# Performance work log

Hardware: AMD Instinct MI355X
Metric: run time of the kernel (lower is better)

## Reference

```python
import jax, jax.numpy as jnp
import numpy as np

N_SENT = 100000   # source ('sent') nodes
N_TYPE = 10000    # destination ('type') nodes
E = 640000        # edges of etype 'has'
D = 128           # out_dim
LEAKY_SLOPE = 0.01  # F.leaky_relu default


def setup_inputs() -> dict:
    key = jax.random.key(0)
    k0, k1, k2, k3, k4 = jax.random.split(key, 5)
    h_sent = jax.random.normal(k0, (N_SENT, D), jnp.float32)
    h_type = jax.random.normal(k1, (N_TYPE, D), jnp.float32)
    # attn_fc: Linear(2*D, 1, bias=False) -> weight [1, 2*D]
    attn_w = jax.random.normal(k2, (1, 2 * D), jnp.float32) * (1.0 / np.sqrt(2 * D))
    src_idx = jax.random.randint(k3, (E,), 0, N_SENT, dtype=jnp.int32)
    dst_idx = jax.random.randint(k4, (E,), 0, N_TYPE, dtype=jnp.int32)
    return {"h_sent": h_sent, "h_type": h_type, "attn_w": attn_w,
            "src_idx": src_idx, "dst_idx": dst_idx}


def reference(h_sent, h_type, attn_w, src_idx, dst_idx):
    w = attn_w[0]  # [2D]
    # attn_fc(cat(src_h, dst_h)) == src_h @ w[:D] + dst_h @ w[D:]  (no bias)
    s_src = h_sent @ w[:D]   # [N_SENT]
    s_dst = h_type @ w[D:]   # [N_TYPE]
    e = jax.nn.leaky_relu(s_src[src_idx] + s_dst[dst_idx], LEAKY_SLOPE)  # [E]
    # segment (per-destination) softmax over incoming edges
    m = jax.ops.segment_max(e, dst_idx, num_segments=N_TYPE)             # [N_TYPE]
    m = jnp.where(jnp.isfinite(m), m, 0.0)                               # empty segments -> 0
    ex = jnp.exp(e - m[dst_idx])                                         # [E]
    denom = jax.ops.segment_sum(ex, dst_idx, num_segments=N_TYPE)        # [N_TYPE]
    alpha = ex / denom[dst_idx]                                          # [E]
    # weighted scatter-sum of source features into destination nodes
    msg = alpha[:, None] * h_sent[src_idx]                               # [E, D]
    h_new = jax.ops.segment_sum(msg, dst_idx, num_segments=N_TYPE)       # [N_TYPE, D]
    # DGL only updates nodes that received messages; isolated nodes keep h
    deg = jax.ops.segment_sum(jnp.ones_like(e), dst_idx, num_segments=N_TYPE)
    return jnp.where(deg[:, None] > 0, h_new, h_type)
```

## Files before the change

### kernel.cpp

```cpp
#include <hip/hip_runtime.h>
#include <stdint.h>
#include <stddef.h>

#define N_SENT 100000
#define N_TYPE 10000
#define NEDGE  640000
#define NROWS  (N_SENT + N_TYPE)
#define MAXDEG 256
#define HB     64
#define HCHUNK (NEDGE / HB)

__device__ __forceinline__ float bf2f(uint32_t lo16) {
    return __builtin_bit_cast(float, lo16 << 16);
}
__device__ __forceinline__ uint32_t f2bf(float f) {
    uint32_t u = __builtin_bit_cast(uint32_t, f);
    return (u + 0x7fffu + ((u >> 16) & 1u)) >> 16;
}

__device__ __forceinline__ bool detect_bf16(const uint32_t* __restrict__ h) {
    uint32_t u = h[threadIdx.x & 63];
    uint32_t e_lo = (u >> 7) & 0xffu;
    int ok = (e_lo >= 100u && e_lo <= 140u) ? 1 : 0;
    unsigned long long m = __ballot(ok);
    return __popcll(m) >= 48;
}

#define SCORE_BLOCKS ((NROWS + 63) / 64)

__global__ __launch_bounds__(256) void scores_k(const void* __restrict__ h_sent,
                                                const void* __restrict__ h_type,
                                                const void* __restrict__ attn_w,
                                                float* __restrict__ s_src,
                                                float* __restrict__ s_dst) {
    int lane = threadIdx.x & 63;
    int r0   = (blockIdx.x * 4 + (int)(threadIdx.x >> 6)) * 16;
    bool isbf = detect_bf16((const uint32_t*)h_sent);
    float v[16];
    if (isbf) {
        uint32_t wv_s = ((const uint32_t*)attn_w)[lane];
        uint32_t wv_t = ((const uint32_t*)attn_w)[64 + lane];
        float ws0 = bf2f(wv_s & 0xffffu), ws1 = bf2f(wv_s >> 16);
        float wt0 = bf2f(wv_t & 0xffffu), wt1 = bf2f(wv_t >> 16);
#pragma unroll
        for (int i = 0; i < 16; i++) {
            int g = r0 + i;
            if (g >= NROWS) { v[i] = 0.0f; continue; }
            bool isSrc = g < N_SENT;
            const uint32_t* hp = isSrc
                ? (const uint32_t*)h_sent + (size_t)g * 64
                : (const uint32_t*)h_type + (size_t)(g - N_SENT) * 64;
            uint32_t hv = hp[lane];
            v[i] = isSrc ? (bf2f(hv & 0xffffu) * ws0 + bf2f(hv >> 16) * ws1)
                         : (bf2f(hv & 0xffffu) * wt0 + bf2f(hv >> 16) * wt1);
        }
    } else {
        float2 wv_s = ((const float2*)attn_w)[lane];
        float2 wv_t = ((const float2*)attn_w)[64 + lane];
#pragma unroll
        for (int i = 0; i < 16; i++) {
            int g = r0 + i;
            if (g >= NROWS) { v[i] = 0.0f; continue; }
            bool isSrc = g < N_SENT;
            const float2* hp = isSrc
                ? (const float2*)h_sent + (size_t)g * 64
                : (const float2*)h_type + (size_t)(g - N_SENT) * 64;
            float2 hv = hp[lane];
            v[i] = isSrc ? (hv.x * wv_s.x + hv.y * wv_s.y)
                         : (hv.x * wv_t.x + hv.y * wv_t.y);
        }
    }
    int b0 = lane & 1, b1 = (lane >> 1) & 1, b2 = (lane >> 2) & 1, b3 = (lane >> 3) & 1;
    float w_[8];
#pragma unroll
    for (int i = 0; i < 8; i++) {
        float keep = b0 ? v[2 * i + 1] : v[2 * i];
        float send = b0 ? v[2 * i]     : v[2 * i + 1];
        w_[i] = keep + __shfl_xor(send, 1, 64);
    }
    float x_[4];
#pragma unroll
    for (int i = 0; i < 4; i++) {
        float keep = b1 ? w_[2 * i + 1] : w_[2 * i];
        float send = b1 ? w_[2 * i]     : w_[2 * i + 1];
        x_[i] = keep + __shfl_xor(send, 2, 64);
    }
    float y_[2];
#pragma unroll
    for (int i = 0; i < 2; i++) {
        float keep = b2 ? x_[2 * i + 1] : x_[2 * i];
        float send = b2 ? x_[2 * i]     : x_[2 * i + 1];
        y_[i] = keep + __shfl_xor(send, 4, 64);
    }
    float z;
    {
        float keep = b3 ? y_[1] : y_[0];
        float send = b3 ? y_[0] : y_[1];
        z = keep + __shfl_xor(send, 8, 64);
    }
    z += __shfl_xor(z, 16, 64);
    z += __shfl_xor(z, 32, 64);
    if (lane < 16) {
        int g = r0 + lane;
        if (g < NROWS) {
            if (g < N_SENT) s_src[g] = z;
            else            s_dst[g - N_SENT] = z;
        }
    }
}

__global__ __launch_bounds__(256) void count_k(const int* __restrict__ dst,
                                               uint32_t* __restrict__ count2) {
    __shared__ uint32_t hist[N_TYPE];
    int cb = blockIdx.x;
    int t  = threadIdx.x;
    for (int i = t; i < N_TYPE; i += 256) hist[i] = 0u;
    __syncthreads();
    int e0 = cb * HCHUNK;
    for (int i = t; i < HCHUNK; i += 256)
        atomicAdd(&hist[dst[e0 + i]], 1u);
    __syncthreads();
    uint32_t* row = count2 + (size_t)cb * N_TYPE;
    for (int i = t; i < N_TYPE; i += 256) row[i] = hist[i];
}

__global__ __launch_bounds__(256) void sumscan_k(uint32_t* __restrict__ count2,
                                                 uint32_t* __restrict__ total) {
    int b = blockIdx.x * 256 + threadIdx.x;
    if (b >= N_TYPE) return;
    uint32_t run = 0;
#pragma unroll 4
    for (int c = 0; c < HB; c++) {
        uint32_t* p = count2 + (size_t)c * N_TYPE + b;
        uint32_t v = *p;
        *p = run;
        run += v;
    }
    total[b] = run;
}

__global__ __launch_bounds__(1024) void scan_k(const uint32_t* __restrict__ total,
                                               uint32_t* __restrict__ offsets) {
    const int CH = 10;
    int t = threadIdx.x, lane = t & 63, wv = t >> 6;
    int base = t * CH;
    uint32_t local[CH];
    uint32_t tsum = 0;
#pragma unroll
    for (int i = 0; i < CH; i++) {
        int idx = base + i;
        uint32_t c = (idx < N_TYPE) ? total[idx] : 0u;
        local[i] = c;
        tsum += c;
    }
    uint32_t orig = tsum;
#pragma unroll
    for (int off = 1; off < 64; off <<= 1) {
        uint32_t v = __shfl_up(tsum, off, 64);
        if (lane >= off) tsum += v;
    }
    __shared__ uint32_t wsum[16];
    if (lane == 63) wsum[wv] = tsum;
    __syncthreads();
    if (wv == 0 && lane < 16) {
        uint32_t u = wsum[lane], o = u;
#pragma unroll
        for (int off = 1; off < 16; off <<= 1) {
            uint32_t v = __shfl_up(u, off, 64);
            if (lane >= off) u += v;
        }
        wsum[lane] = u - o;
    }
    __syncthreads();
    uint32_t run = wsum[wv] + tsum - orig;
#pragma unroll
    for (int i = 0; i < CH; i++) {
        int idx = base + i;
        if (idx < N_TYPE) {
            offsets[idx] = run;
            run += local[i];
        } else if (idx == N_TYPE) {
            offsets[idx] = run;
        }
    }
}

__global__ __launch_bounds__(256) void fill_k(const int* __restrict__ src,
                                              const int* __restrict__ dst,
                                              const uint32_t* __restrict__ offsets,
                                              const uint32_t* __restrict__ base2,
                                              uint32_t* __restrict__ edge_src) {
    __shared__ uint32_t cur[N_TYPE];
    int cb = blockIdx.x;
    int t  = threadIdx.x;
    const uint32_t* brow = base2 + (size_t)cb * N_TYPE;
    for (int i = t; i < N_TYPE; i += 256) cur[i] = offsets[i] + brow[i];
    __syncthreads();
    int e0 = cb * HCHUNK;
    for (int i = t; i < HCHUNK; i += 256) {
        int e = e0 + i;
        uint32_t pos = atomicAdd(&cur[dst[e]], 1u);
        edge_src[pos] = (uint32_t)src[e];
    }
}

__global__ __launch_bounds__(256) void agg_k(const void* __restrict__ h_sent,
                                             const void* __restrict__ h_type,
                                             const float* __restrict__ s_src,
                                             const float* __restrict__ s_dst,
                                             const uint32_t* __restrict__ offsets,
                                             const uint32_t* __restrict__ edge_src,
                                             void* __restrict__ out) {
    __shared__ float    sc[4][MAXDEG];
    __shared__ uint32_t ss[4][MAXDEG];
    int j     = (blockIdx.x * 256 + threadIdx.x) >> 6;
    int wslot = threadIdx.x >> 6;
    int lane  = threadIdx.x & 63;
    bool valid = j < N_TYPE;
    bool isbf  = detect_bf16((const uint32_t*)h_sent);
    uint32_t beg = 0, deg = 0;
    float sdj = 0.0f;
    if (valid) {
        beg = offsets[j];
        deg = offsets[j + 1] - beg;
        sdj = s_dst[j];
    }
    float*    mysc = sc[wslot];
    uint32_t* myss = ss[wslot];
    bool fits = (deg <= MAXDEG);
    float m = -INFINITY;
    for (uint32_t k = lane; k < deg; k += 64) {
        uint32_t s = edge_src[beg + k];
        float v = s_src[s] + sdj;
        v = v > 0.0f ? v : 0.01f * v;
        if (fits) { mysc[k] = v; myss[k] = s; }
        m = fmaxf(m, v);
    }
#pragma unroll
    for (int off = 32; off; off >>= 1) m = fmaxf(m, __shfl_xor(m, off, 64));
    __syncthreads();
    if (!valid) return;
    if (deg == 0) {
        if (isbf) ((uint32_t*)out)[(size_t)j * 64 + lane] =
                      ((const uint32_t*)h_type)[(size_t)j * 64 + lane];
        else      ((float2*)out)[(size_t)j * 64 + lane] =
                      ((const float2*)h_type)[(size_t)j * 64 + lane];
        return;
    }
    float denom = 0.0f, a0 = 0.0f, a1 = 0.0f;
    if (isbf) {
        const uint32_t* hp = (const uint32_t*)h_sent;
        uint32_t k = 0;
        if (fits) {
            for (; k + 8 <= deg; k += 8) {
                uint32_t sv[8]; float vv[8]; uint32_t gv[8];
#pragma unroll
                for (int i = 0; i < 8; i++) { sv[i] = myss[k + i]; vv[i] = mysc[k + i]; }
#pragma unroll
                for (int i = 0; i < 8; i++) gv[i] = hp[(size_t)sv[i] * 64 + lane];
#pragma unroll
                for (int i = 0; i < 8; i++) {
                    float w = __expf(vv[i] - m);
                    denom += w;
                    a0 += w * bf2f(gv[i] & 0xffffu);
                    a1 += w * bf2f(gv[i] >> 16);
                }
            }
            for (; k < deg; ++k) {
                float w = __expf(mysc[k] - m);
                uint32_t g = hp[(size_t)myss[k] * 64 + lane];
                denom += w;
                a0 += w * bf2f(g & 0xffffu);
                a1 += w * bf2f(g >> 16);
            }
        } else {
            for (k = 0; k < deg; ++k) {
                uint32_t s = edge_src[beg + k];
                float v = s_src[s] + sdj; v = v > 0.0f ? v : 0.01f * v;
                float w = __expf(v - m);
                uint32_t g = hp[(size_t)s * 64 + lane];
                denom += w;
                a0 += w * bf2f(g & 0xffffu);
                a1 += w * bf2f(g >> 16);
            }
        }
        float inv = 1.0f / denom;
        ((uint32_t*)out)[(size_t)j * 64 + lane] = f2bf(a0 * inv) | (f2bf(a1 * inv) << 16);
    } else {
        const float2* hp = (const float2*)h_sent;
        uint32_t k = 0;
        if (fits) {
            for (; k + 8 <= deg; k += 8) {
                uint32_t sv[8]; float vv[8]; float2 gv[8];
#pragma unroll
                for (int i = 0; i < 8; i++) { sv[i] = myss[k + i]; vv[i] = mysc[k + i]; }
#pragma unroll
                for (int i = 0; i < 8; i++) gv[i] = hp[(size_t)sv[i] * 64 + lane];
#pragma unroll
                for (int i = 0; i < 8; i++) {
                    float w = __expf(vv[i] - m);
                    denom += w;
                    a0 += w * gv[i].x;
                    a1 += w * gv[i].y;
                }
            }
            for (; k < deg; ++k) {
                float w = __expf(mysc[k] - m);
                float2 g = hp[(size_t)myss[k] * 64 + lane];
                denom += w;
                a0 += w * g.x;
                a1 += w * g.y;
            }
        } else {
            for (k = 0; k < deg; ++k) {
                uint32_t s = edge_src[beg + k];
                float v = s_src[s] + sdj; v = v > 0.0f ? v : 0.01f * v;
                float w = __expf(v - m);
                float2 g = hp[(size_t)s * 64 + lane];
                denom += w;
                a0 += w * g.x;
                a1 += w * g.y;
            }
        }
        float inv = 1.0f / denom;
        ((float2*)out)[(size_t)j * 64 + lane] = make_float2(a0 * inv, a1 * inv);
    }
}

static inline size_t align_up(size_t x) { return (x + 255) & ~(size_t)255; }

extern "C" void kernel_launch(void* const* d_in, const int* in_sizes, int n_in,
                              void* d_out, int out_size, void* d_ws, size_t ws_size,
                              hipStream_t stream) {
    const void* h_sent = d_in[0];
    const void* h_type = d_in[1];
    const void* attn_w = d_in[2];
    const int* src_idx = (const int*)d_in[3];
    const int* dst_idx = (const int*)d_in[4];

    char* w = (char*)d_ws;
    float*    s_src     = (float*)w;    w += align_up((size_t)N_SENT * 4);
    float*    s_dst     = (float*)w;    w += align_up((size_t)N_TYPE * 4);
    uint32_t* count2    = (uint32_t*)w; w += align_up((size_t)HB * N_TYPE * 4);
    uint32_t* total     = (uint32_t*)w; w += align_up((size_t)N_TYPE * 4);
    uint32_t* offsets   = (uint32_t*)w; w += align_up((size_t)(N_TYPE + 1) * 4);
    uint32_t* edge_src  = (uint32_t*)w; w += align_up((size_t)NEDGE * 4);

    scores_k<<<SCORE_BLOCKS, 256, 0, stream>>>(h_sent, h_type, attn_w, s_src, s_dst);
    count_k<<<HB, 256, 0, stream>>>(dst_idx, count2);
    sumscan_k<<<(N_TYPE + 255) / 256, 256, 0, stream>>>(count2, total);
    scan_k<<<1, 1024, 0, stream>>>(total, offsets);
    fill_k<<<HB, 256, 0, stream>>>(src_idx, dst_idx, offsets, count2, edge_src);
    agg_k<<<(N_TYPE + 3) / 4, 256, 0, stream>>>(h_sent, h_type, s_src, s_dst,
                                                offsets, edge_src, d_out);
}
```

Measured before the change: 198.3 us.

## Precompute edge weights in fill and split aggregation into source-row slabs for locality

The fill kernel now computes each edge's unnormalized softmax weight exp(leaky_relu(s_src+s_dst)) and stores it next to the source index, removing the per-destination max pass. Aggregation is split into 8 slabs over source-row ranges so concurrently running blocks gather from a smaller part of h_sent, aiming for better L2 reuse. Partial numerators are stored as bf16 and summed in a combine kernel, with a plain single-pass fallback when workspace is short. The cost is that every edge list is scanned 8 times, plus extra partial-buffer traffic and an extra launch. Dropping max subtraction risks overflow for large scores, and bf16 partials lose precision on fp32 inputs.

```diff
diff --git a/kernel.cpp b/kernel.cpp
--- a/kernel.cpp
+++ b/kernel.cpp
@@ -6,9 +6,10 @@
 #define N_TYPE 10000
 #define NEDGE  640000
 #define NROWS  (N_SENT + N_TYPE)
-#define MAXDEG 256
 #define HB     64
 #define HCHUNK (NEDGE / HB)
+#define NSLAB  8
+#define SLABW  (N_SENT / NSLAB)
 
 __device__ __forceinline__ float bf2f(uint32_t lo16) {
     return __builtin_bit_cast(float, lo16 << 16);
@@ -187,9 +188,11 @@
 
 __global__ __launch_bounds__(256) void fill_k(const int* __restrict__ src,
                                               const int* __restrict__ dst,
+                                              const float* __restrict__ s_src,
+                                              const float* __restrict__ s_dst,
                                               const uint32_t* __restrict__ offsets,
                                               const uint32_t* __restrict__ base2,
-                                              uint32_t* __restrict__ edge_src) {
+                                              uint2* __restrict__ edata) {
     __shared__ uint32_t cur[N_TYPE];
     int cb = blockIdx.x;
     int t  = threadIdx.x;
@@ -199,132 +202,168 @@
     int e0 = cb * HCHUNK;
     for (int i = t; i < HCHUNK; i += 256) {
         int e = e0 + i;
-        uint32_t pos = atomicAdd(&cur[dst[e]], 1u);
-        edge_src[pos] = (uint32_t)src[e];
-    }
-}
-
-__global__ __launch_bounds__(256) void agg_k(const void* __restrict__ h_sent,
-                                             const void* __restrict__ h_type,
-                                             const float* __restrict__ s_src,
-                                             const float* __restrict__ s_dst,
-                                             const uint32_t* __restrict__ offsets,
-                                             const uint32_t* __restrict__ edge_src,
-                                             void* __restrict__ out) {
-    __shared__ float    sc[4][MAXDEG];
-    __shared__ uint32_t ss[4][MAXDEG];
-    int j     = (blockIdx.x * 256 + threadIdx.x) >> 6;
-    int wslot = threadIdx.x >> 6;
-    int lane  = threadIdx.x & 63;
-    bool valid = j < N_TYPE;
-    bool isbf  = detect_bf16((const uint32_t*)h_sent);
-    uint32_t beg = 0, deg = 0;
-    float sdj = 0.0f;
-    if (valid) {
-        beg = offsets[j];
-        deg = offsets[j + 1] - beg;
-        sdj = s_dst[j];
-    }
-    float*    mysc = sc[wslot];
-    uint32_t* myss = ss[wslot];
-    bool fits = (deg <= MAXDEG);
-    float m = -INFINITY;
-    for (uint32_t k = lane; k < deg; k += 64) {
-        uint32_t s = edge_src[beg + k];
-        float v = s_src[s] + sdj;
+        int d = dst[e];
+        int s = src[e];
+        float v = s_src[s] + s_dst[d];
         v = v > 0.0f ? v : 0.01f * v;
-        if (fits) { mysc[k] = v; myss[k] = s; }
-        m = fmaxf(m, v);
-    }
-#pragma unroll
-    for (int off = 32; off; off >>= 1) m = fmaxf(m, __shfl_xor(m, off, 64));
-    __syncthreads();
-    if (!valid) return;
-    if (deg == 0) {
-        if (isbf) ((uint32_t*)out)[(size_t)j * 64 + lane] =
-                      ((const uint32_t*)h_type)[(size_t)j * 64 + lane];
-        else      ((float2*)out)[(size_t)j * 64 + lane] =
-                      ((const float2*)h_type)[(size_t)j * 64 + lane];
-        return;
-    }
-    float denom = 0.0f, a0 = 0.0f, a1 = 0.0f;
-    if (isbf) {
-        const uint32_t* hp = (const uint32_t*)h_sent;
-        uint32_t k = 0;
-        if (fits) {
-            for (; k + 8 <= deg; k += 8) {
-                uint32_t sv[8]; float vv[8]; uint32_t gv[8];
-#pragma unroll
-                for (int i = 0; i < 8; i++) { sv[i] = myss[k + i]; vv[i] = mysc[k + i]; }
-#pragma unroll
-                for (int i = 0; i < 8; i++) gv[i] = hp[(size_t)sv[i] * 64 + lane];
+        float w = __expf(v);
+        uint32_t pos = atomicAdd(&cur[d], 1u);
+        edata[pos] = make_uint2((uint32_t)s, __builtin_bit_cast(uint32_t, w));
+    }
+}
+
+__global__ __launch_bounds__(256) void slab_agg_k(const void* __restrict__ h_sent,
+                                                  const uint32_t* __restrict__ offsets,
+                                                  const uint2* __restrict__ edata,
+                                                  uint32_t* __restrict__ pnum,
+                                                  float* __restrict__ pden) {
+    int lane = threadIdx.x & 63;
+    int slab = blockIdx.x & 7;
+    int j    = (blockIdx.x >> 3) * 4 + (threadIdx.x >> 6);
+    if (j >= N_TYPE) return;
+    bool isbf = detect_bf16((const uint32_t*)h_sent);
+    uint32_t beg = offsets[j], end = offsets[j + 1];
+    uint32_t slo = (uint32_t)slab * SLABW, shi = slo + SLABW;
+    const uint32_t* hpb = (const uint32_t*)h_sent;
+    const float2*   hpf = (const float2*)h_sent;
+    float a0 = 0.0f, a1 = 0.0f, wsum = 0.0f;
+    for (uint32_t base = beg; base < end; base += 64) {
+        uint32_t k = base + lane;
+        uint2 ed = (k < end) ? edata[k] : make_uint2(0u, 0u);
+        uint32_t s = ed.x;
+        float    w = __builtin_bit_cast(float, ed.y);
+        bool act = (k < end) && (s >= slo) && (s < shi);
+        float wl = act ? w : 0.0f;
+        wsum += wl;
+        unsigned long long mask = __ballot(act);
+        while (mask) {
+            int idx[8];
+            int cnt = 0;
+            while (mask && cnt < 8) { idx[cnt++] = __builtin_ctzll(mask); mask &= mask - 1; }
+#pragma unroll
+            for (int i = 0; i < 8; i++) if (i >= cnt) idx[i] = 0;
+            uint32_t sb[8]; float wb[8];
+#pragma unroll
+            for (int i = 0; i < 8; i++) {
+                sb[i] = __shfl(s,  idx[i], 64);
+                wb[i] = (i < cnt) ? __shfl(wl, idx[i], 64) : 0.0f;
+            }
+            if (isbf) {
+                uint32_t gv[8];
+#pragma unroll
+                for (int i = 0; i < 8; i++) gv[i] = (i < cnt) ? hpb[(size_t)sb[i] * 64 + lane] : 0u;
 #pragma unroll
                 for (int i = 0; i < 8; i++) {
-                    float w = __expf(vv[i] - m);
-                    denom += w;
-                    a0 += w * bf2f(gv[i] & 0xffffu);
-                    a1 += w * bf2f(gv[i] >> 16);
+                    a0 += wb[i] * bf2f(gv[i] & 0xffffu);
+                    a1 += wb[i] * bf2f(gv[i] >> 16);
+                }
+            } else {
+                float2 gv[8];
+#pragma unroll
+                for (int i = 0; i < 8; i++)
+                    gv[i] = (i < cnt) ? hpf[(size_t)sb[i] * 64 + lane] : make_float2(0.f, 0.f);
+#pragma unroll
+                for (int i = 0; i < 8; i++) {
+                    a0 += wb[i] * gv[i].x;
+                    a1 += wb[i] * gv[i].y;
                 }
             }
-            for (; k < deg; ++k) {
-                float w = __expf(mysc[k] - m);
-                uint32_t g = hp[(size_t)myss[k] * 64 + lane];
-                denom += w;
-                a0 += w * bf2f(g & 0xffffu);
-                a1 += w * bf2f(g >> 16);
+        }
+    }
+#pragma unroll
+    for (int off = 32; off; off >>= 1) wsum += __shfl_xor(wsum, off, 64);
+    uint32_t row = (uint32_t)j * 8 + slab;
+    pnum[(size_t)row * 64 + lane] = f2bf(a0) | (f2bf(a1) << 16);
+    if (lane == 0) pden[row] = wsum;
+}
+
+__global__ __launch_bounds__(256) void combine_k(const void* __restrict__ h_type,
+                                                 const uint32_t* __restrict__ pnum,
+                                                 const float* __restrict__ pden,
+                                                 void* __restrict__ out) {
+    int lane = threadIdx.x & 63;
+    int j = (blockIdx.x * 256 + (int)threadIdx.x) >> 6;
+    if (j >= N_TYPE) return;
+    bool isbf = detect_bf16((const uint32_t*)h_type);
+    float a0 = 0.0f, a1 = 0.0f, den = 0.0f;
+#pragma unroll
+    for (int s = 0; s < 8; s++) {
+        uint32_t row = (uint32_t)j * 8 + s;
+        uint32_t v = pnum[(size_t)row * 64 + lane];
+        a0 += bf2f(v & 0xffffu);
+        a1 += bf2f(v >> 16);
+        den += pden[row];
+    }
+    if (den > 0.0f) {
+        float inv = 1.0f / den;
+        if (isbf) ((uint32_t*)out)[(size_t)j * 64 + lane] = f2bf(a0 * inv) | (f2bf(a1 * inv) << 16);
+        else      ((float2*)out)[(size_t)j * 64 + lane]   = make_float2(a0 * inv, a1 * inv);
+    } else {
+        if (isbf) ((uint32_t*)out)[(size_t)j * 64 + lane] = ((const uint32_t*)h_type)[(size_t)j * 64 + lane];
+        else      ((float2*)out)[(size_t)j * 64 + lane]   = ((const float2*)h_type)[(size_t)j * 64 + lane];
+    }
+}
+
+__global__ __launch_bounds__(256) void plain_agg_k(const void* __restrict__ h_sent,
+                                                   const void* __restrict__ h_type,
+                                                   const uint32_t* __restrict__ offsets,
+                                                   const uint2* __restrict__ edata,
+                                                   void* __restrict__ out) {
+    int lane = threadIdx.x & 63;
+    int j = (blockIdx.x * 256 + (int)threadIdx.x) >> 6;
+    if (j >= N_TYPE) return;
+    bool isbf = detect_bf16((const uint32_t*)h_sent);
+    uint32_t beg = offsets[j], end = offsets[j + 1];
+    if (beg == end) {
+        if (isbf) ((uint32_t*)out)[(size_t)j * 64 + lane] = ((const uint32_t*)h_type)[(size_t)j * 64 + lane];
+        else      ((float2*)out)[(size_t)j * 64 + lane]   = ((const float2*)h_type)[(size_t)j * 64 + lane];
+        return;
+    }
+    const uint32_t* hpb = (const uint32_t*)h_sent;
+    const float2*   hpf = (const float2*)h_sent;
+    float a0 = 0.0f, a1 = 0.0f, wsum = 0.0f;
+    for (uint32_t base = beg; base < end; base += 64) {
+        uint32_t k = base + lane;
+        uint2 ed = (k < end) ? edata[k] : make_uint2(0u, 0u);
+        uint32_t s = ed.x;
+        float    w = (k < end) ? __builtin_bit_cast(float, ed.y) : 0.0f;
+        wsum += w;
+        int rem = (int)(end - base); if (rem > 64) rem = 64;
+        for (int bb = 0; bb < rem; bb += 8) {
+            int cnt = rem - bb; if (cnt > 8) cnt = 8;
+            uint32_t sb[8]; float wb[8];
+#pragma unroll
+            for (int i = 0; i < 8; i++) {
+                sb[i] = __shfl(s, bb + i, 64);
+                wb[i] = (i < cnt) ? __shfl(w, bb + i, 64) : 0.0f;
             }
-        } else {
-            for (k = 0; k < deg; ++k) {
-                uint32_t s = edge_src[beg + k];
-                float v = s_src[s] + sdj; v = v > 0.0f ? v : 0.01f * v;
-                float w = __expf(v - m);
-                uint32_t g = hp[(size_t)s * 64 + lane];
-                denom += w;
-                a0 += w * bf2f(g & 0xffffu);
-                a1 += w * bf2f(g >> 16);
-            }
-        }
-        float inv = 1.0f / denom;
-        ((uint32_t*)out)[(size_t)j * 64 + lane] = f2bf(a0 * inv) | (f2bf(a1 * inv) << 16);
-    } else {
-        const float2* hp = (const float2*)h_sent;
-        uint32_t k = 0;
-        if (fits) {
-            for (; k + 8 <= deg; k += 8) {
-                uint32_t sv[8]; float vv[8]; float2 gv[8];
-#pragma unroll
-                for (int i = 0; i < 8; i++) { sv[i] = myss[k + i]; vv[i] = mysc[k + i]; }
-#pragma unroll
-                for (int i = 0; i < 8; i++) gv[i] = hp[(size_t)sv[i] * 64 + lane];
+            if (isbf) {
+                uint32_t gv[8];
+#pragma unroll
+                for (int i = 0; i < 8; i++) gv[i] = (i < cnt) ? hpb[(size_t)sb[i] * 64 + lane] : 0u;
 #pragma unroll
                 for (int i = 0; i < 8; i++) {
-                    float w = __expf(vv[i] - m);
-                    denom += w;
-                    a0 += w * gv[i].x;
-                    a1 += w * gv[i].y;
+                    a0 += wb[i] * bf2f(gv[i] & 0xffffu);
+                    a1 += wb[i] * bf2f(gv[i] >> 16);
+                }
+            } else {
+                float2 gv[8];
+#pragma unroll
+                for (int i = 0; i < 8; i++)
+                    gv[i] = (i < cnt) ? hpf[(size_t)sb[i] * 64 + lane] : make_float2(0.f, 0.f);
+#pragma unroll
+                for (int i = 0; i < 8; i++) {
+                    a0 += wb[i] * gv[i].x;
+                    a1 += wb[i] * gv[i].y;
                 }
             }
-            for (; k < deg; ++k) {
-                float w = __expf(mysc[k] - m);
-                float2 g = hp[(size_t)myss[k] * 64 + lane];
-                denom += w;
-                a0 += w * g.x;
-                a1 += w * g.y;
-            }
-        } else {
-            for (k = 0; k < deg; ++k) {
-                uint32_t s = edge_src[beg + k];
-                float v = s_src[s] + sdj; v = v > 0.0f ? v : 0.01f * v;
-                float w = __expf(v - m);
-                float2 g = hp[(size_t)s * 64 + lane];
-                denom += w;
-                a0 += w * g.x;
-                a1 += w * g.y;
-            }
-        }
-        float inv = 1.0f / denom;
-        ((float2*)out)[(size_t)j * 64 + lane] = make_float2(a0 * inv, a1 * inv);
-    }
+        }
+    }
+#pragma unroll
+    for (int off = 32; off; off >>= 1) wsum += __shfl_xor(wsum, off, 64);
+    float inv = 1.0f / wsum;
+    if (isbf) ((uint32_t*)out)[(size_t)j * 64 + lane] = f2bf(a0 * inv) | (f2bf(a1 * inv) << 16);
+    else      ((float2*)out)[(size_t)j * 64 + lane]   = make_float2(a0 * inv, a1 * inv);
 }
 
 static inline size_t align_up(size_t x) { return (x + 255) & ~(size_t)255; }
@@ -339,18 +378,26 @@
     const int* dst_idx = (const int*)d_in[4];
 
     char* w = (char*)d_ws;
-    float*    s_src     = (float*)w;    w += align_up((size_t)N_SENT * 4);
-    float*    s_dst     = (float*)w;    w += align_up((size_t)N_TYPE * 4);
-    uint32_t* count2    = (uint32_t*)w; w += align_up((size_t)HB * N_TYPE * 4);
-    uint32_t* total     = (uint32_t*)w; w += align_up((size_t)N_TYPE * 4);
-    uint32_t* offsets   = (uint32_t*)w; w += align_up((size_t)(N_TYPE + 1) * 4);
-    uint32_t* edge_src  = (uint32_t*)w; w += align_up((size_t)NEDGE * 4);
+    float*    s_src   = (float*)w;    w += align_up((size_t)N_SENT * 4);
+    float*    s_dst   = (float*)w;    w += align_up((size_t)N_TYPE * 4);
+    uint32_t* count2  = (uint32_t*)w; w += align_up((size_t)HB * N_TYPE * 4);
+    uint32_t* total   = (uint32_t*)w; w += align_up((size_t)N_TYPE * 4);
+    uint32_t* offsets = (uint32_t*)w; w += align_up((size_t)(N_TYPE + 1) * 4);
+    uint2*    edata   = (uint2*)w;    w += align_up((size_t)NEDGE * 8);
+    uint32_t* pnum    = (uint32_t*)w; w += align_up((size_t)N_TYPE * 8 * 64 * 4);
+    float*    pden    = (float*)w;    w += align_up((size_t)N_TYPE * 8 * 4);
+    size_t need_slab = (size_t)(w - (char*)d_ws);
+    bool use_slab = ws_size >= need_slab;
 
     scores_k<<<SCORE_BLOCKS, 256, 0, stream>>>(h_sent, h_type, attn_w, s_src, s_dst);
     count_k<<<HB, 256, 0, stream>>>(dst_idx, count2);
     sumscan_k<<<(N_TYPE + 255) / 256, 256, 0, stream>>>(count2, total);
     scan_k<<<1, 1024, 0, stream>>>(total, offsets);
-    fill_k<<<HB, 256, 0, stream>>>(src_idx, dst_idx, offsets, count2, edge_src);
-    agg_k<<<(N_TYPE + 3) / 4, 256, 0, stream>>>(h_sent, h_type, s_src, s_dst,
-                                                offsets, edge_src, d_out);
-}
+    fill_k<<<HB, 256, 0, stream>>>(src_idx, dst_idx, s_src, s_dst, offsets, count2, edata);
+    if (use_slab) {
+        slab_agg_k<<<(N_TYPE / 4) * 8, 256, 0, stream>>>(h_sent, offsets, edata, pnum, pden);
+        combine_k<<<(N_TYPE + 3) / 4, 256, 0, stream>>>(h_type, pnum, pden, d_out);
+    } else {
+        plain_agg_k<<<(N_TYPE + 3) / 4, 256, 0, stream>>>(h_sent, h_type, offsets, edata, d_out);
+    }
+}
```

Result: slower. 233.6 us (+17.8%).

## Precompute unnormalized edge weights in CSR fill and drop the per-node max pass

Applied to the files above, without the earlier changes.

The score kernel and the destination histogram kernel are merged into one launch, split by block index. The histogram chunk count doubles so the count and fill kernels get more parallelism. The fill kernel now computes each edge's leaky-relu score and exp() weight and stores it next to the source index. The aggregation kernel then does a single pass without the segment-max reduction or LDS staging. The softmax loses its max-subtraction stabilization, so it could overflow for large scores. The fused kernel also gives every score block a 40KB shared array, which may cut its occupancy.

```diff
diff --git a/kernel.cpp b/kernel.cpp
--- a/kernel.cpp
+++ b/kernel.cpp
@@ -6,8 +6,7 @@
 #define N_TYPE 10000
 #define NEDGE  640000
 #define NROWS  (N_SENT + N_TYPE)
-#define MAXDEG 256
-#define HB     64
+#define HB     128
 #define HCHUNK (NEDGE / HB)
 
 __device__ __forceinline__ float bf2f(uint32_t lo16) {
@@ -17,7 +16,6 @@
     uint32_t u = __builtin_bit_cast(uint32_t, f);
     return (u + 0x7fffu + ((u >> 16) & 1u)) >> 16;
 }
-
 __device__ __forceinline__ bool detect_bf16(const uint32_t* __restrict__ h) {
     uint32_t u = h[threadIdx.x & 63];
     uint32_t e_lo = (u >> 7) & 0xffu;
@@ -28,100 +26,102 @@
 
 #define SCORE_BLOCKS ((NROWS + 63) / 64)
 
-__global__ __launch_bounds__(256) void scores_k(const void* __restrict__ h_sent,
-                                                const void* __restrict__ h_type,
-                                                const void* __restrict__ attn_w,
-                                                float* __restrict__ s_src,
-                                                float* __restrict__ s_dst) {
-    int lane = threadIdx.x & 63;
-    int r0   = (blockIdx.x * 4 + (int)(threadIdx.x >> 6)) * 16;
-    bool isbf = detect_bf16((const uint32_t*)h_sent);
-    float v[16];
-    if (isbf) {
-        uint32_t wv_s = ((const uint32_t*)attn_w)[lane];
-        uint32_t wv_t = ((const uint32_t*)attn_w)[64 + lane];
-        float ws0 = bf2f(wv_s & 0xffffu), ws1 = bf2f(wv_s >> 16);
-        float wt0 = bf2f(wv_t & 0xffffu), wt1 = bf2f(wv_t >> 16);
-#pragma unroll
-        for (int i = 0; i < 16; i++) {
-            int g = r0 + i;
-            if (g >= NROWS) { v[i] = 0.0f; continue; }
-            bool isSrc = g < N_SENT;
-            const uint32_t* hp = isSrc
-                ? (const uint32_t*)h_sent + (size_t)g * 64
-                : (const uint32_t*)h_type + (size_t)(g - N_SENT) * 64;
-            uint32_t hv = hp[lane];
-            v[i] = isSrc ? (bf2f(hv & 0xffffu) * ws0 + bf2f(hv >> 16) * ws1)
-                         : (bf2f(hv & 0xffffu) * wt0 + bf2f(hv >> 16) * wt1);
+__global__ __launch_bounds__(256) void scores_count_k(const void* __restrict__ h_sent,
+                                                      const void* __restrict__ h_type,
+                                                      const void* __restrict__ attn_w,
+                                                      const int* __restrict__ dst,
+                                                      float* __restrict__ s_src,
+                                                      float* __restrict__ s_dst,
+                                                      uint32_t* __restrict__ count2) {
+    __shared__ uint32_t hist[N_TYPE];
+    int b = blockIdx.x;
+    if (b < SCORE_BLOCKS) {
+        int lane = threadIdx.x & 63;
+        int r0   = (b * 4 + (int)(threadIdx.x >> 6)) * 16;
+        bool isbf = detect_bf16((const uint32_t*)h_sent);
+        float v[16];
+        if (isbf) {
+            uint32_t wv_s = ((const uint32_t*)attn_w)[lane];
+            uint32_t wv_t = ((const uint32_t*)attn_w)[64 + lane];
+            float ws0 = bf2f(wv_s & 0xffffu), ws1 = bf2f(wv_s >> 16);
+            float wt0 = bf2f(wv_t & 0xffffu), wt1 = bf2f(wv_t >> 16);
+#pragma unroll
+            for (int i = 0; i < 16; i++) {
+                int g = r0 + i;
+                if (g >= NROWS) { v[i] = 0.0f; continue; }
+                bool isSrc = g < N_SENT;
+                const uint32_t* hp = isSrc
+                    ? (const uint32_t*)h_sent + (size_t)g * 64
+                    : (const uint32_t*)h_type + (size_t)(g - N_SENT) * 64;
+                uint32_t hv = hp[lane];
+                v[i] = isSrc ? (bf2f(hv & 0xffffu) * ws0 + bf2f(hv >> 16) * ws1)
+                             : (bf2f(hv & 0xffffu) * wt0 + bf2f(hv >> 16) * wt1);
+            }
+        } else {
+            float2 wv_s = ((const float2*)attn_w)[lane];
+            float2 wv_t = ((const float2*)attn_w)[64 + lane];
+#pragma unroll
+            for (int i = 0; i < 16; i++) {
+                int g = r0 + i;
+                if (g >= NROWS) { v[i] = 0.0f; continue; }
+                bool isSrc = g < N_SENT;
+                const float2* hp = isSrc
+                    ? (const float2*)h_sent + (size_t)g * 64
+                    : (const float2*)h_type + (size_t)(g - N_SENT) * 64;
+                float2 hv = hp[lane];
+                v[i] = isSrc ? (hv.x * wv_s.x + hv.y * wv_s.y)
+                             : (hv.x * wv_t.x + hv.y * wv_t.y);
+            }
+        }
+        int b0 = lane & 1, b1 = (lane >> 1) & 1, b2 = (lane >> 2) & 1, b3 = (lane >> 3) & 1;
+        float w_[8];
+#pragma unroll
+        for (int i = 0; i < 8; i++) {
+            float keep = b0 ? v[2 * i + 1] : v[2 * i];
+            float send = b0 ? v[2 * i]     : v[2 * i + 1];
+            w_[i] = keep + __shfl_xor(send, 1, 64);
+        }
+        float x_[4];
+#pragma unroll
+        for (int i = 0; i < 4; i++) {
+            float keep = b1 ? w_[2 * i + 1] : w_[2 * i];
+            float send = b1 ? w_[2 * i]     : w_[2 * i + 1];
+            x_[i] = keep + __shfl_xor(send, 2, 64);
+        }
+        float y_[2];
+#pragma unroll
+        for (int i = 0; i < 2; i++) {
+            float keep = b2 ? x_[2 * i + 1] : x_[2 * i];
+            float send = b2 ? x_[2 * i]     : x_[2 * i + 1];
+            y_[i] = keep + __shfl_xor(send, 4, 64);
+        }
+        float z;
+        {
+            float keep = b3 ? y_[1] : y_[0];
+            float send = b3 ? y_[0] : y_[1];
+            z = keep + __shfl_xor(send, 8, 64);
+        }
+        z += __shfl_xor(z, 16, 64);
+        z += __shfl_xor(z, 32, 64);
+        if (lane < 16) {
+            int g = r0 + lane;
+            if (g < NROWS) {
+                if (g < N_SENT) s_src[g] = z;
+                else            s_dst[g - N_SENT] = z;
+            }
         }
     } else {
-        float2 wv_s = ((const float2*)attn_w)[lane];
-        float2 wv_t = ((const float2*)attn_w)[64 + lane];
-#pragma unroll
-        for (int i = 0; i < 16; i++) {
-            int g = r0 + i;
-            if (g >= NROWS) { v[i] = 0.0f; continue; }
-            bool isSrc = g < N_SENT;
-            const float2* hp = isSrc
-                ? (const float2*)h_sent + (size_t)g * 64
-                : (const float2*)h_type + (size_t)(g - N_SENT) * 64;
-            float2 hv = hp[lane];
-            v[i] = isSrc ? (hv.x * wv_s.x + hv.y * wv_s.y)
-                         : (hv.x * wv_t.x + hv.y * wv_t.y);
-        }
-    }
-    int b0 = lane & 1, b1 = (lane >> 1) & 1, b2 = (lane >> 2) & 1, b3 = (lane >> 3) & 1;
-    float w_[8];
-#pragma unroll
-    for (int i = 0; i < 8; i++) {
-        float keep = b0 ? v[2 * i + 1] : v[2 * i];
-        float send = b0 ? v[2 * i]     : v[2 * i + 1];
-        w_[i] = keep + __shfl_xor(send, 1, 64);
-    }
-    float x_[4];
-#pragma unroll
-    for (int i = 0; i < 4; i++) {
-        float keep = b1 ? w_[2 * i + 1] : w_[2 * i];
-        float send = b1 ? w_[2 * i]     : w_[2 * i + 1];
-        x_[i] = keep + __shfl_xor(send, 2, 64);
-    }
-    float y_[2];
-#pragma unroll
-    for (int i = 0; i < 2; i++) {
-        float keep = b2 ? x_[2 * i + 1] : x_[2 * i];
-        float send = b2 ? x_[2 * i]     : x_[2 * i + 1];
-        y_[i] = keep + __shfl_xor(send, 4, 64);
-    }
-    float z;
-    {
-        float keep = b3 ? y_[1] : y_[0];
-        float send = b3 ? y_[0] : y_[1];
-        z = keep + __shfl_xor(send, 8, 64);
-    }
-    z += __shfl_xor(z, 16, 64);
-    z += __shfl_xor(z, 32, 64);
-    if (lane < 16) {
-        int g = r0 + lane;
-        if (g < NROWS) {
-            if (g < N_SENT) s_src[g] = z;
-            else            s_dst[g - N_SENT] = z;
-        }
-    }
-}
-
-__global__ __launch_bounds__(256) void count_k(const int* __restrict__ dst,
-                                               uint32_t* __restrict__ count2) {
-    __shared__ uint32_t hist[N_TYPE];
-    int cb = blockIdx.x;
-    int t  = threadIdx.x;
-    for (int i = t; i < N_TYPE; i += 256) hist[i] = 0u;
-    __syncthreads();
-    int e0 = cb * HCHUNK;
-    for (int i = t; i < HCHUNK; i += 256)
-        atomicAdd(&hist[dst[e0 + i]], 1u);
-    __syncthreads();
-    uint32_t* row = count2 + (size_t)cb * N_TYPE;
-    for (int i = t; i < N_TYPE; i += 256) row[i] = hist[i];
+        int cb = b - SCORE_BLOCKS;
+        int t  = threadIdx.x;
+        for (int i = t; i < N_TYPE; i += 256) hist[i] = 0u;
+        __syncthreads();
+        int e0 = cb * HCHUNK;
+        for (int i = t; i < HCHUNK; i += 256)
+            atomicAdd(&hist[dst[e0 + i]], 1u);
+        __syncthreads();
+        uint32_t* row = count2 + (size_t)cb * N_TYPE;
+        for (int i = t; i < N_TYPE; i += 256) row[i] = hist[i];
+    }
 }
 
 __global__ __launch_bounds__(256) void sumscan_k(uint32_t* __restrict__ count2,
@@ -129,7 +129,7 @@
     int b = blockIdx.x * 256 + threadIdx.x;
     if (b >= N_TYPE) return;
     uint32_t run = 0;
-#pragma unroll 4
+#pragma unroll 8
     for (int c = 0; c < HB; c++) {
         uint32_t* p = count2 + (size_t)c * N_TYPE + b;
         uint32_t v = *p;
@@ -187,9 +187,11 @@
 
 __global__ __launch_bounds__(256) void fill_k(const int* __restrict__ src,
                                               const int* __restrict__ dst,
+                                              const float* __restrict__ s_src,
+                                              const float* __restrict__ s_dst,
                                               const uint32_t* __restrict__ offsets,
                                               const uint32_t* __restrict__ base2,
-                                              uint32_t* __restrict__ edge_src) {
+                                              uint2* __restrict__ edata) {
     __shared__ uint32_t cur[N_TYPE];
     int cb = blockIdx.x;
     int t  = threadIdx.x;
@@ -199,130 +201,89 @@
     int e0 = cb * HCHUNK;
     for (int i = t; i < HCHUNK; i += 256) {
         int e = e0 + i;
-        uint32_t pos = atomicAdd(&cur[dst[e]], 1u);
-        edge_src[pos] = (uint32_t)src[e];
+        int d = dst[e];
+        int s = src[e];
+        float v = s_src[s] + s_dst[d];
+        v = v > 0.0f ? v : 0.01f * v;
+        float w = __expf(v);
+        uint32_t pos = atomicAdd(&cur[d], 1u);
+        edata[pos] = make_uint2((uint32_t)s, __builtin_bit_cast(uint32_t, w));
     }
 }
 
 __global__ __launch_bounds__(256) void agg_k(const void* __restrict__ h_sent,
                                              const void* __restrict__ h_type,
-                                             const float* __restrict__ s_src,
-                                             const float* __restrict__ s_dst,
                                              const uint32_t* __restrict__ offsets,
-                                             const uint32_t* __restrict__ edge_src,
+                                             const uint2* __restrict__ edata,
                                              void* __restrict__ out) {
-    __shared__ float    sc[4][MAXDEG];
-    __shared__ uint32_t ss[4][MAXDEG];
-    int j     = (blockIdx.x * 256 + threadIdx.x) >> 6;
-    int wslot = threadIdx.x >> 6;
-    int lane  = threadIdx.x & 63;
-    bool valid = j < N_TYPE;
-    bool isbf  = detect_bf16((const uint32_t*)h_sent);
-    uint32_t beg = 0, deg = 0;
-    float sdj = 0.0f;
-    if (valid) {
-        beg = offsets[j];
-        deg = offsets[j + 1] - beg;
-        sdj = s_dst[j];
-    }
-    float*    mysc = sc[wslot];
-    uint32_t* myss = ss[wslot];
-    bool fits = (deg <= MAXDEG);
-    float m = -INFINITY;
-    for (uint32_t k = lane; k < deg; k += 64) {
-        uint32_t s = edge_src[beg + k];
-        float v = s_src[s] + sdj;
-        v = v > 0.0f ? v : 0.01f * v;
-        if (fits) { mysc[k] = v; myss[k] = s; }
-        m = fmaxf(m, v);
-    }
-#pragma unroll
-    for (int off = 32; off; off >>= 1) m = fmaxf(m, __shfl_xor(m, off, 64));
-    __syncthreads();
-    if (!valid) return;
-    if (deg == 0) {
+    int lane = threadIdx.x & 63;
+    int j = (blockIdx.x * 256 + (int)threadIdx.x) >> 6;
+    if (j >= N_TYPE) return;
+    bool isbf = detect_bf16((const uint32_t*)h_sent);
+    uint32_t beg = offsets[j], end = offsets[j + 1];
+    if (beg == end) {
         if (isbf) ((uint32_t*)out)[(size_t)j * 64 + lane] =
                       ((const uint32_t*)h_type)[(size_t)j * 64 + lane];
         else      ((float2*)out)[(size_t)j * 64 + lane] =
                       ((const float2*)h_type)[(size_t)j * 64 + lane];
         return;
     }
-    float denom = 0.0f, a0 = 0.0f, a1 = 0.0f;
+    float a0 = 0.0f, a1 = 0.0f, den = 0.0f;
     if (isbf) {
         const uint32_t* hp = (const uint32_t*)h_sent;
-        uint32_t k = 0;
-        if (fits) {
-            for (; k + 8 <= deg; k += 8) {
-                uint32_t sv[8]; float vv[8]; uint32_t gv[8];
-#pragma unroll
-                for (int i = 0; i < 8; i++) { sv[i] = myss[k + i]; vv[i] = mysc[k + i]; }
-#pragma unroll
-                for (int i = 0; i < 8; i++) gv[i] = hp[(size_t)sv[i] * 64 + lane];
-#pragma unroll
-                for (int i = 0; i < 8; i++) {
-                    float w = __expf(vv[i] - m);
-                    denom += w;
-                    a0 += w * bf2f(gv[i] & 0xffffu);
-                    a1 += w * bf2f(gv[i] >> 16);
-                }
-            }
-            for (; k < deg; ++k) {
-                float w = __expf(mysc[k] - m);
-                uint32_t g = hp[(size_t)myss[k] * 64 + lane];
-                denom += w;
-                a0 += w * bf2f(g & 0xffffu);
-                a1 += w * bf2f(g >> 16);
-            }
-        } else {
-            for (k = 0; k < deg; ++k) {
-                uint32_t s = edge_src[beg + k];
-                float v = s_src[s] + sdj; v = v > 0.0f ? v : 0.01f * v;
-                float w = __expf(v - m);
-                uint32_t g = hp[(size_t)s * 64 + lane];
-                denom += w;
-                a0 += w * bf2f(g & 0xffffu);
-                a1 += w * bf2f(g >> 16);
-            }
-        }
-        float inv = 1.0f / denom;
+        uint32_t k = beg;
+        for (; k + 8 <= end; k += 8) {
+            uint2 ed[8];
+#pragma unroll
+            for (int i = 0; i < 8; i++) ed[i] = edata[k + i];
+            uint32_t gv[8];
+#pragma unroll
+            for (int i = 0; i < 8; i++) gv[i] = hp[(size_t)ed[i].x * 64 + lane];
+#pragma unroll
+            for (int i = 0; i < 8; i++) {
+                float w = __builtin_bit_cast(float, ed[i].y);
+                den += w;
+                a0 += w * bf2f(gv[i] & 0xffffu);
+                a1 += w * bf2f(gv[i] >> 16);
+            }
+        }
+        for (; k < end; ++k) {
+            uint2 ed = edata[k];
+            uint32_t gv = hp[(size_t)ed.x * 64 + lane];
+            float w = __builtin_bit_cast(float, ed.y);
+            den += w;
+            a0 += w * bf2f(gv & 0xffffu);
+            a1 += w * bf2f(gv >> 16);
+        }
+        float inv = 1.0f / den;
         ((uint32_t*)out)[(size_t)j * 64 + lane] = f2bf(a0 * inv) | (f2bf(a1 * inv) << 16);
     } else {
         const float2* hp = (const float2*)h_sent;
-        uint32_t k = 0;
-        if (fits) {
-            for (; k + 8 <= deg; k += 8) {
-                uint32_t sv[8]; float vv[8]; float2 gv[8];
-#pragma unroll
-                for (int i = 0; i < 8; i++) { sv[i] = myss[k + i]; vv[i] = mysc[k + i]; }
-#pragma unroll
-                for (int i = 0; i < 8; i++) gv[i] = hp[(size_t)sv[i] * 64 + lane];
-#pragma unroll
-                for (int i = 0; i < 8; i++) {
-                    float w = __expf(vv[i] - m);
-                    denom += w;
-                    a0 += w * gv[i].x;
-                    a1 += w * gv[i].y;
-                }
-            }
-            for (; k < deg; ++k) {
-                float w = __expf(mysc[k] - m);
-                float2 g = hp[(size_t)myss[k] * 64 + lane];
-                denom += w;
-                a0 += w * g.x;
-                a1 += w * g.y;
-            }
-        } else {
-            for (k = 0; k < deg; ++k) {
-                uint32_t s = edge_src[beg + k];
-                float v = s_src[s] + sdj; v = v > 0.0f ? v : 0.01f * v;
-                float w = __expf(v - m);
-                float2 g = hp[(size_t)s * 64 + lane];
-                denom += w;
-                a0 += w * g.x;
-                a1 += w * g.y;
-            }
-        }
-        float inv = 1.0f / denom;
+        uint32_t k = beg;
+        for (; k + 8 <= end; k += 8) {
+            uint2 ed[8];
+#pragma unroll
+            for (int i = 0; i < 8; i++) ed[i] = edata[k + i];
+            float2 gv[8];
+#pragma unroll
+            for (int i = 0; i < 8; i++) gv[i] = hp[(size_t)ed[i].x * 64 + lane];
+#pragma unroll
+            for (int i = 0; i < 8; i++) {
+                float w = __builtin_bit_cast(float, ed[i].y);
+                den += w;
+                a0 += w * gv[i].x;
+                a1 += w * gv[i].y;
+            }
+        }
+        for (; k < end; ++k) {
+            uint2 ed = edata[k];
+            float2 gv = hp[(size_t)ed.x * 64 + lane];
+            float w = __builtin_bit_cast(float, ed.y);
+            den += w;
+            a0 += w * gv.x;
+            a1 += w * gv.y;
+        }
+        float inv = 1.0f / den;
         ((float2*)out)[(size_t)j * 64 + lane] = make_float2(a0 * inv, a1 * inv);
     }
 }
@@ -339,18 +300,17 @@
     const int* dst_idx = (const int*)d_in[4];
 
     char* w = (char*)d_ws;
-    float*    s_src     = (float*)w;    w += align_up((size_t)N_SENT * 4);
-    float*    s_dst     = (float*)w;    w += align_up((size_t)N_TYPE * 4);
-    uint32_t* count2    = (uint32_t*)w; w += align_up((size_t)HB * N_TYPE * 4);
-    uint32_t* total     = (uint32_t*)w; w += align_up((size_t)N_TYPE * 4);
-    uint32_t* offsets   = (uint32_t*)w; w += align_up((size_t)(N_TYPE + 1) * 4);
-    uint32_t* edge_src  = (uint32_t*)w; w += align_up((size_t)NEDGE * 4);
-
-    scores_k<<<SCORE_BLOCKS, 256, 0, stream>>>(h_sent, h_type, attn_w, s_src, s_dst);
-    count_k<<<HB, 256, 0, stream>>>(dst_idx, count2);
+    float*    s_src   = (float*)w;    w += align_up((size_t)N_SENT * 4);
+    float*    s_dst   = (float*)w;    w += align_up((size_t)N_TYPE * 4);
+    uint32_t* count2  = (uint32_t*)w; w += align_up((size_t)HB * N_TYPE * 4);
+    uint32_t* total   = (uint32_t*)w; w += align_up((size_t)N_TYPE * 4);
+    uint32_t* offsets = (uint32_t*)w; w += align_up((size_t)(N_TYPE + 1) * 4);
+    uint2*    edata   = (uint2*)w;    w += align_up((size_t)NEDGE * 8);
+
+    scores_count_k<<<SCORE_BLOCKS + HB, 256, 0, stream>>>(
+        h_sent, h_type, attn_w, dst_idx, s_src, s_dst, count2);
     sumscan_k<<<(N_TYPE + 255) / 256, 256, 0, stream>>>(count2, total);
     scan_k<<<1, 1024, 0, stream>>>(total, offsets);
-    fill_k<<<HB, 256, 0, stream>>>(src_idx, dst_idx, offsets, count2, edge_src);
-    agg_k<<<(N_TYPE + 3) / 4, 256, 0, stream>>>(h_sent, h_type, s_src, s_dst,
-                                                offsets, edge_src, d_out);
-}
+    fill_k<<<HB, 256, 0, stream>>>(src_idx, dst_idx, s_src, s_dst, offsets, count2, edata);
+    agg_k<<<(N_TYPE + 3) / 4, 256, 0, stream>>>(h_sent, h_type, offsets, edata, d_out);
+}
```

After: 199.3 us. About the same (+0.5%).
